# Kernel tuning notes

Hardware: AMD Instinct MI355X
Metric: run time of the kernel (lower is better)

The kernel has to match this reference:

```python
import jax, jax.numpy as jnp
import numpy as np

T, B, E, H, HID, SIG = 1024, 4, 1024, 16, 1024, 64


def setup_inputs() -> dict:
    key = jax.random.key(0)
    ks = jax.random.split(key, 16)
    sc = 0.02
    return {
        "x": jax.random.normal(ks[0], (T, B, E), jnp.float32),
        "Wq": jax.random.normal(ks[1], (E, E), jnp.float32) * sc,
        "bq": jnp.zeros((E,), jnp.float32),
        "Wk": jax.random.normal(ks[2], (E, E), jnp.float32) * sc,
        "bk": jnp.zeros((E,), jnp.float32),
        "Wv": jax.random.normal(ks[3], (E, E), jnp.float32) * sc,
        "bv": jnp.zeros((E,), jnp.float32),
        "Wo": jax.random.normal(ks[4], (E, E), jnp.float32) * sc,
        "bo": jnp.zeros((E,), jnp.float32),
        "W1": jax.random.normal(ks[5], (HID, E), jnp.float32) * sc,
        "b1": jnp.zeros((HID,), jnp.float32),
        "W2": jax.random.normal(ks[6], (SIG, HID), jnp.float32) * sc,
        "b2": jnp.zeros((SIG,), jnp.float32),
        "head_signatures": jax.random.normal(ks[7], (H, SIG), jnp.float32),
    }


def reference(x, Wq, bq, Wk, bk, Wv, bv, Wo, bo, W1, b1, W2, b2, head_signatures):
    # x: (T, B, E) fairseq layout; self-attention, no mask, eval mode (no dropout)
    T_, B_, E_ = x.shape
    H_ = head_signatures.shape[0]
    d = E_ // H_
    scaling = d ** -0.5

    q = (x @ Wq.T + bq) * scaling            # (T,B,E)
    k = x @ Wk.T + bk
    v = x @ Wv.T + bv

    def split_heads(z):                        # (T,B,E) -> (B,H,T,d)
        return z.reshape(T_, B_, H_, d).transpose(1, 2, 0, 3)

    qh, kh, vh = split_heads(q), split_heads(k), split_heads(v)

    scores = jnp.einsum("bhtd,bhsd->bhts", qh, kh)   # (B,H,T,T)
    attn = jax.nn.softmax(scores, axis=-1)
    o = jnp.einsum("bhts,bhsd->bhtd", attn, vh)      # (B,H,T,d)

    # head-competition gate: signature MLP on x, match against head signatures,
    # softmax over heads ('softmax' competition type)
    t = jax.nn.relu(x @ W1.T + b1) @ W2.T + b2       # (T,B,SIG)
    logits = t @ head_signatures.T                   # (T,B,H)
    gate = jax.nn.softmax(logits, axis=-1)
    gate = gate.transpose(1, 2, 0)                   # (B,H,T)

    o = o * gate[..., None]                          # gate per-head outputs
    out = o.transpose(2, 0, 1, 3).reshape(T_, B_, E_)  # (T,B,E)
    return out @ Wo.T + bo
```

## Files before the change

### kernel.cpp

```cpp
#include <hip/hip_runtime.h>

#define Tn   1024
#define Bn   4
#define En   1024
#define Hn   16
#define HIDn 1024
#define SIGn 64
#define Mn   (Tn * Bn)

typedef short  s8x8  __attribute__((ext_vector_type(8)));
typedef float  f32x4 __attribute__((ext_vector_type(4)));

__device__ __forceinline__ float bf2f(unsigned short u) {
    return __uint_as_float(((unsigned int)u) << 16);
}
__device__ __forceinline__ unsigned short f2bf(float f) {
    unsigned int x = __float_as_uint(f);
    unsigned int r = (x + 0x7fffu + ((x >> 16) & 1u)) >> 16;
    return (unsigned short)r;
}
__device__ __forceinline__ float exp2asm(float x) {
    float r;
    asm("v_exp_f32 %0, %1" : "=v"(r) : "v"(x));
    return r;
}
__device__ __forceinline__ unsigned int cvtpk(float a, float b) {
    unsigned int r;
    asm("v_cvt_pk_bf16_f32 %0, %1, %2" : "=v"(r) : "v"(a), "v"(b));
    return r;
}

__device__ __forceinline__ void gload_lds16(const void* g, void* l) {
    __builtin_amdgcn_global_load_lds(
        (const __attribute__((address_space(1))) unsigned int*)g,
        (__attribute__((address_space(3))) unsigned int*)l, 16, 0, 0);
}

__global__ __launch_bounds__(256) void cast_bf16(
    const float* __restrict__ s, unsigned short* __restrict__ d, int n8)
{
    int i = blockIdx.x * 256 + threadIdx.x;
    if (i >= n8) return;
    const float4* p = (const float4*)(s + (size_t)i * 8);
    float4 a = p[0], b = p[1];
    s8x8 o;
    o[0] = (short)f2bf(a.x); o[1] = (short)f2bf(a.y);
    o[2] = (short)f2bf(a.z); o[3] = (short)f2bf(a.w);
    o[4] = (short)f2bf(b.x); o[5] = (short)f2bf(b.y);
    o[6] = (short)f2bf(b.z); o[7] = (short)f2bf(b.w);
    *(s8x8*)(d + (size_t)i * 8) = o;
}

__global__ __launch_bounds__(256) void cast_w4(
    const float* __restrict__ W1, const float* __restrict__ Wq,
    const float* __restrict__ Wk, const float* __restrict__ Wv,
    unsigned short* __restrict__ Wcat)
{
    const size_t WELEM = (size_t)En * En;
    int y = blockIdx.y;
    const float* src = (y == 0) ? W1 : (y == 1) ? Wq : (y == 2) ? Wk : Wv;
    unsigned short* dst = Wcat + (size_t)y * WELEM;
    int i = blockIdx.x * 256 + threadIdx.x;
    const float4* p = (const float4*)(src + (size_t)i * 8);
    float4 a = p[0], b = p[1];
    s8x8 o;
    o[0] = (short)f2bf(a.x); o[1] = (short)f2bf(a.y);
    o[2] = (short)f2bf(a.z); o[3] = (short)f2bf(a.w);
    o[4] = (short)f2bf(b.x); o[5] = (short)f2bf(b.y);
    o[6] = (short)f2bf(b.z); o[7] = (short)f2bf(b.w);
    *(s8x8*)(dst + (size_t)i * 8) = o;
}

__global__ __launch_bounds__(256) void bias_concat(
    const float* __restrict__ b1, const float* __restrict__ bq,
    const float* __restrict__ bk, const float* __restrict__ bv,
    float* __restrict__ bcat)
{
    int i = blockIdx.x * 256 + threadIdx.x;
    int w = i >> 10;
    const float* s = (w == 0) ? b1 : (w == 1) ? bq : (w == 2) ? bk : bv;
    bcat[i] = s[i & 1023];
}

template <int PRE>
__global__ __launch_bounds__(256) void fused_proj(
    const float* __restrict__ X, const unsigned short* __restrict__ Xb,
    const unsigned short* __restrict__ Wcat, const float* __restrict__ bcat,
    unsigned short* __restrict__ t1b, unsigned short* __restrict__ qb,
    unsigned short* __restrict__ kb, unsigned short* __restrict__ vb)
{
    __shared__ __align__(16) short As[128 * 32];
    __shared__ __align__(16) short Bs[128 * 32];
    const int tid  = threadIdx.x;
    const int wave = tid >> 6;
    const int lane = tid & 63;
    const int ln15 = lane & 15;
    const int kq   = lane >> 4;
    const int wr   = wave >> 1;
    const int wc   = wave & 1;
    const int bn   = blockIdx.x;
    const int bm   = blockIdx.y;
    const size_t rowA0 = (size_t)bm * 128;
    const size_t rowB0 = (size_t)bn * 128;

    const int lrow   = lane >> 2;
    const int lchunk = lane & 3;

    f32x4 acc[4][4];
#pragma unroll
    for (int m = 0; m < 4; m++)
#pragma unroll
        for (int n = 0; n < 4; n++) acc[m][n] = (f32x4){0.f, 0.f, 0.f, 0.f};

    for (int k0 = 0; k0 < 1024; k0 += 32) {
#pragma unroll
        for (int i = 0; i < 2; i++) {
            int row = wave * 32 + i * 16 + lrow;
            int c   = lchunk ^ ((row >> 1) & 3);
            gload_lds16(Wcat + (rowB0 + row) * 1024 + k0 + c * 8,
                        &Bs[(wave * 32 + i * 16) * 32]);
        }
        if (PRE) {
#pragma unroll
            for (int i = 0; i < 2; i++) {
                int row = wave * 32 + i * 16 + lrow;
                int c   = lchunk ^ ((row >> 1) & 3);
                gload_lds16(Xb + (rowA0 + row) * 1024 + k0 + c * 8,
                            &As[(wave * 32 + i * 16) * 32]);
            }
        } else {
            const int srow = tid >> 1;
            const int scol = (tid & 1) * 16;
            const float4* src = (const float4*)(X + (rowA0 + srow) * 1024 + k0 + scol);
            float4 a = src[0], b = src[1], c4 = src[2], d4 = src[3];
            s8x8 v0, v1;
            v0[0] = (short)f2bf(a.x);  v0[1] = (short)f2bf(a.y);
            v0[2] = (short)f2bf(a.z);  v0[3] = (short)f2bf(a.w);
            v0[4] = (short)f2bf(b.x);  v0[5] = (short)f2bf(b.y);
            v0[6] = (short)f2bf(b.z);  v0[7] = (short)f2bf(b.w);
            v1[0] = (short)f2bf(c4.x); v1[1] = (short)f2bf(c4.y);
            v1[2] = (short)f2bf(c4.z); v1[3] = (short)f2bf(c4.w);
            v1[4] = (short)f2bf(d4.x); v1[5] = (short)f2bf(d4.y);
            v1[6] = (short)f2bf(d4.z); v1[7] = (short)f2bf(d4.w);
            int sw = (srow >> 1) & 3;
            int c0 = (scol >> 3) ^ sw;
            int c1 = ((scol >> 3) + 1) ^ sw;
            *(s8x8*)&As[srow * 32 + c0 * 8] = v0;
            *(s8x8*)&As[srow * 32 + c1 * 8] = v1;
        }
        asm volatile("s_waitcnt vmcnt(0)" ::: "memory");
        __syncthreads();

        s8x8 af[4], bf[4];
#pragma unroll
        for (int m = 0; m < 4; m++) {
            int row = wr * 64 + m * 16 + ln15;
            af[m] = *(const s8x8*)&As[row * 32 + (kq ^ ((row >> 1) & 3)) * 8];
        }
#pragma unroll
        for (int n = 0; n < 4; n++) {
            int row = wc * 64 + n * 16 + ln15;
            bf[n] = *(const s8x8*)&Bs[row * 32 + (kq ^ ((row >> 1) & 3)) * 8];
        }
#pragma unroll
        for (int m = 0; m < 4; m++)
#pragma unroll
            for (int n = 0; n < 4; n++)
                acc[m][n] = __builtin_amdgcn_mfma_f32_16x16x32_bf16(
                    af[m], bf[n], acc[m][n], 0, 0, 0);
        __syncthreads();
    }

    const int which = bn >> 3;
    unsigned short* dst = (which == 0) ? t1b : (which == 1) ? qb
                        : (which == 2) ? kb : vb;
    const float scale = (which == 1) ? 0.18033688011112042f : 1.0f;
    const int   relu  = (which == 0);
    const int   cbase = (bn & 7) * 128;

    float bcol[4];
#pragma unroll
    for (int n = 0; n < 4; n++)
        bcol[n] = bcat[bn * 128 + wc * 64 + n * 16 + ln15];
#pragma unroll
    for (int m = 0; m < 4; m++) {
        size_t gr0 = rowA0 + wr * 64 + m * 16 + kq * 4;
#pragma unroll
        for (int n = 0; n < 4; n++) {
            int gc = cbase + wc * 64 + n * 16 + ln15;
#pragma unroll
            for (int j = 0; j < 4; j++) {
                float vv = acc[m][n][j] + bcol[n];
                if (relu) vv = fmaxf(vv, 0.f);
                vv *= scale;
                dst[(gr0 + j) * 1024 + gc] = f2bf(vv);
            }
        }
    }
}

__global__ __launch_bounds__(256) void out_proj(
    const unsigned short* __restrict__ A, const unsigned short* __restrict__ W,
    const float* __restrict__ bias, float* __restrict__ C)
{
    __shared__ __align__(16) short As[64 * 32];
    __shared__ __align__(16) short Bs[128 * 32];
    const int tid  = threadIdx.x;
    const int wave = tid >> 6;
    const int lane = tid & 63;
    const int ln15 = lane & 15;
    const int kq   = lane >> 4;
    const int wr   = wave >> 1;
    const int wc   = wave & 1;
    const size_t rowA0 = (size_t)blockIdx.y * 64;
    const size_t rowB0 = (size_t)blockIdx.x * 128;

    const int lrow   = lane >> 2;
    const int lchunk = lane & 3;

    f32x4 acc[2][4];
#pragma unroll
    for (int m = 0; m < 2; m++)
#pragma unroll
        for (int n = 0; n < 4; n++) acc[m][n] = (f32x4){0.f, 0.f, 0.f, 0.f};

    for (int k0 = 0; k0 < 1024; k0 += 32) {
        {
            int row = wave * 16 + lrow;
            int c   = lchunk ^ ((row >> 1) & 3);
            gload_lds16(A + (rowA0 + row) * 1024 + k0 + c * 8,
                        &As[(wave * 16) * 32]);
        }
#pragma unroll
        for (int i = 0; i < 2; i++) {
            int row = wave * 32 + i * 16 + lrow;
            int c   = lchunk ^ ((row >> 1) & 3);
            gload_lds16(W + (rowB0 + row) * 1024 + k0 + c * 8,
                        &Bs[(wave * 32 + i * 16) * 32]);
        }
        asm volatile("s_waitcnt vmcnt(0)" ::: "memory");
        __syncthreads();

        s8x8 af[2], bf[4];
#pragma unroll
        for (int m = 0; m < 2; m++) {
            int row = wr * 32 + m * 16 + ln15;
            af[m] = *(const s8x8*)&As[row * 32 + (kq ^ ((row >> 1) & 3)) * 8];
        }
#pragma unroll
        for (int n = 0; n < 4; n++) {
            int row = wc * 64 + n * 16 + ln15;
            bf[n] = *(const s8x8*)&Bs[row * 32 + (kq ^ ((row >> 1) & 3)) * 8];
        }
#pragma unroll
        for (int m = 0; m < 2; m++)
#pragma unroll
            for (int n = 0; n < 4; n++)
                acc[m][n] = __builtin_amdgcn_mfma_f32_16x16x32_bf16(
                    af[m], bf[n], acc[m][n], 0, 0, 0);
        __syncthreads();
    }

    float bcol[4];
#pragma unroll
    for (int n = 0; n < 4; n++)
        bcol[n] = bias[rowB0 + wc * 64 + n * 16 + ln15];
#pragma unroll
    for (int m = 0; m < 2; m++) {
        size_t gr0 = rowA0 + wr * 32 + m * 16 + kq * 4;
#pragma unroll
        for (int n = 0; n < 4; n++) {
            size_t gc = rowB0 + wc * 64 + n * 16 + ln15;
#pragma unroll
            for (int j = 0; j < 4; j++)
                C[(gr0 + j) * 1024 + gc] = acc[m][n][j] + bcol[n];
        }
    }
}

__global__ __launch_bounds__(256) void t2gate(
    const unsigned short* __restrict__ t1, const unsigned short* __restrict__ W2b,
    const float* __restrict__ b2, const float* __restrict__ hs,
    float* __restrict__ gate)
{
    __shared__ __align__(16) short As[16 * 32];
    __shared__ __align__(16) short Bs[64 * 32];
    __shared__ float t2s[16][65];
    __shared__ float hss[16][65];
    const int tid  = threadIdx.x;
    const int wave = tid >> 6;
    const int lane = tid & 63;
    const int ln15 = lane & 15;
    const int kq   = lane >> 4;
    const int m0   = blockIdx.x * 16;

    {
        int r = tid >> 4, c = (tid & 15) * 4;
        float4 v = *(const float4*)(hs + r * 64 + c);
        hss[r][c] = v.x; hss[r][c + 1] = v.y; hss[r][c + 2] = v.z; hss[r][c + 3] = v.w;
    }

    f32x4 acc = (f32x4){0.f, 0.f, 0.f, 0.f};
    for (int k0 = 0; k0 < 1024; k0 += 32) {
        if (tid < 64) {
            int row = tid >> 2, ch = tid & 3;
            int cs = ch ^ ((row >> 1) & 3);
            s8x8 vA = *(const s8x8*)(t1 + (size_t)(m0 + row) * 1024 + k0 + ch * 8);
            *(s8x8*)&As[row * 32 + cs * 8] = vA;
        }
        {
            int row = tid >> 2, ch = tid & 3;
            int cs = ch ^ ((row >> 1) & 3);
            s8x8 vB = *(const s8x8*)(W2b + (size_t)row * 1024 + k0 + ch * 8);
            *(s8x8*)&Bs[row * 32 + cs * 8] = vB;
        }
        __syncthreads();
        int arow = ln15;
        int brow = wave * 16 + ln15;
        s8x8 af = *(const s8x8*)&As[arow * 32 + (kq ^ ((arow >> 1) & 3)) * 8];
        s8x8 bf = *(const s8x8*)&Bs[brow * 32 + (kq ^ ((brow >> 1) & 3)) * 8];
        acc = __builtin_amdgcn_mfma_f32_16x16x32_bf16(af, bf, acc, 0, 0, 0);
        __syncthreads();
    }

#pragma unroll
    for (int j = 0; j < 4; j++)
        t2s[kq * 4 + j][wave * 16 + ln15] = acc[j] + b2[wave * 16 + ln15];
    __syncthreads();

    int r = tid >> 4, hd = tid & 15;
    float s = 0.f;
#pragma unroll 16
    for (int d = 0; d < 64; d++) s += t2s[r][d] * hss[hd][d];
    float mx = s;
    mx = fmaxf(mx, __shfl_xor(mx, 1));
    mx = fmaxf(mx, __shfl_xor(mx, 2));
    mx = fmaxf(mx, __shfl_xor(mx, 4));
    mx = fmaxf(mx, __shfl_xor(mx, 8));
    float e = __expf(s - mx);
    float sum = e;
    sum += __shfl_xor(sum, 1);
    sum += __shfl_xor(sum, 2);
    sum += __shfl_xor(sum, 4);
    sum += __shfl_xor(sum, 8);
    gate[(size_t)(m0 + r) * Hn + hd] = e / sum;
}

__global__ __launch_bounds__(256) void transpose_v(
    const unsigned short* __restrict__ vb, unsigned short* __restrict__ vt)
{
    __shared__ unsigned short ts[64][65];
    const int bh = blockIdx.x;
    const int b = bh >> 4, h = bh & 15;
    const int t0 = blockIdx.y * 64;
    const int tid = threadIdx.x;
    {
        int tr = tid >> 2, dq = (tid & 3) * 16;
        const unsigned short* src =
            vb + ((size_t)(t0 + tr) * Bn + b) * En + h * 64 + dq;
        s8x8 a = *(const s8x8*)src;
        s8x8 c = *(const s8x8*)(src + 8);
#pragma unroll
        for (int i = 0; i < 8; i++) {
            ts[tr][dq + i]     = (unsigned short)a[i];
            ts[tr][dq + 8 + i] = (unsigned short)c[i];
        }
    }
    __syncthreads();
    {
        int dr = tid >> 2, tq = (tid & 3) * 16;
        unsigned short* dst = vt + ((size_t)bh * 64 + dr) * Tn + t0 + tq;
        s8x8 o0, o1;
#pragma unroll
        for (int i = 0; i < 8; i++) {
            o0[i] = (short)ts[tq + i][dr];
            o1[i] = (short)ts[tq + 8 + i][dr];
        }
        *(s8x8*)dst = o0;
        *(s8x8*)(dst + 8) = o1;
    }
}

__global__ __launch_bounds__(256, 5) void attn_mfma(
    const unsigned short* __restrict__ q, const unsigned short* __restrict__ k,
    const unsigned short* __restrict__ vt, const float* __restrict__ gate,
    unsigned short* __restrict__ o)
{
    __shared__ __align__(16) short Kls[2][64 * 64];
    __shared__ __align__(16) short Vls[2][64 * 64];

    const int tid  = threadIdx.x;
    const int w    = tid >> 6;
    const int lane = tid & 63;
    const int ln   = lane & 15;
    const int kq   = lane >> 4;
    const int bh   = blockIdx.x;
    const int b    = bh >> 4;
    const int h    = bh & 15;
    const int qt   = blockIdx.y;

    s8x8 qf[2];
    {
        const int qrow = qt * 64 + w * 16 + ln;
        const unsigned short* src =
            q + ((size_t)qrow * Bn + b) * En + h * 64 + kq * 8;
        qf[0] = *(const s8x8*)(src);
        qf[1] = *(const s8x8*)(src + 32);
    }

    f32x4 OT[4];
#pragma unroll
    for (int n = 0; n < 4; n++) OT[n] = (f32x4){0.f, 0.f, 0.f, 0.f};
    float mrun = -1e30f, lrun = 0.f;

    const int srow0 = w * 16 + (lane >> 3);

    auto stage = [&](int bufi, int s0) {
#pragma unroll
        for (int i = 0; i < 2; i++) {
            int row = srow0 + i * 8;
            int c   = (lane & 7) ^ (row & 7);
            int sK  = 32 * (w >> 1) + 4 * (w & 1)
                    + 8 * ((row >> 2) & 3) + (row & 3);
            const unsigned short* gk =
                k + ((size_t)(s0 + sK) * Bn + b) * En + h * 64 + c * 8;
            gload_lds16(gk, &Kls[bufi][w * 1024 + i * 512]);
            const unsigned short* gv =
                vt + ((size_t)bh * 64 + row) * Tn + s0 + c * 8;
            gload_lds16(gv, &Vls[bufi][w * 1024 + i * 512]);
        }
    };

    stage(0, 0);
    asm volatile("s_waitcnt vmcnt(0)" ::: "memory");
    __syncthreads();

    int cur = 0;
    for (int t = 0; t < Tn / 64; t++) {
        if (t + 1 < Tn / 64) stage(cur ^ 1, (t + 1) * 64);

        f32x4 S[4];
#pragma unroll
        for (int n = 0; n < 4; n++) {
            S[n] = (f32x4){0.f, 0.f, 0.f, 0.f};
#pragma unroll
            for (int kk = 0; kk < 2; kk++) {
                int row = n * 16 + ln;
                int cc  = (kk * 4 + kq) ^ (row & 7);
                s8x8 kf = *(const s8x8*)&Kls[cur][row * 64 + cc * 8];
                S[n] = __builtin_amdgcn_mfma_f32_16x16x32_bf16(kf, qf[kk], S[n], 0, 0, 0);
            }
        }

        float rm;
        {
            f32x4 t0 = S[0];
#pragma unroll
            for (int n = 1; n < 4; n++) {
                t0[0] = fmaxf(t0[0], S[n][0]); t0[1] = fmaxf(t0[1], S[n][1]);
                t0[2] = fmaxf(t0[2], S[n][2]); t0[3] = fmaxf(t0[3], S[n][3]);
            }
            rm = fmaxf(fmaxf(t0[0], t0[1]), fmaxf(t0[2], t0[3]));
            rm = fmaxf(rm, __shfl_xor(rm, 16));
            rm = fmaxf(rm, __shfl_xor(rm, 32));
        }

        if (__any(rm > mrun + 8.0f)) {
            float mnew = fmaxf(mrun, rm);
            float fs = exp2asm(mrun - mnew);
            lrun *= fs;
#pragma unroll
            for (int n = 0; n < 4; n++) {
                OT[n][0] *= fs; OT[n][1] *= fs; OT[n][2] *= fs; OT[n][3] *= fs;
            }
            mrun = mnew;
        }

        float ps = 0.f;
#pragma unroll
        for (int n = 0; n < 4; n++) {
            S[n][0] = exp2asm(S[n][0] - mrun); ps += S[n][0];
            S[n][1] = exp2asm(S[n][1] - mrun); ps += S[n][1];
            S[n][2] = exp2asm(S[n][2] - mrun); ps += S[n][2];
            S[n][3] = exp2asm(S[n][3] - mrun); ps += S[n][3];
        }
        ps += __shfl_xor(ps, 16);
        ps += __shfl_xor(ps, 32);
        lrun += ps;

        union { unsigned int u[4]; s8x8 v; } pb[2];
#pragma unroll
        for (int kk = 0; kk < 2; kk++) {
            pb[kk].u[0] = cvtpk(S[2 * kk][0],     S[2 * kk][1]);
            pb[kk].u[1] = cvtpk(S[2 * kk][2],     S[2 * kk][3]);
            pb[kk].u[2] = cvtpk(S[2 * kk + 1][0], S[2 * kk + 1][1]);
            pb[kk].u[3] = cvtpk(S[2 * kk + 1][2], S[2 * kk + 1][3]);
        }

#pragma unroll
        for (int kk = 0; kk < 2; kk++) {
#pragma unroll
            for (int n = 0; n < 4; n++) {
                int row = n * 16 + ln;
                int cv  = (kk * 4 + kq) ^ (row & 7);
                s8x8 vf = *(const s8x8*)&Vls[cur][row * 64 + cv * 8];
                OT[n] = __builtin_amdgcn_mfma_f32_16x16x32_bf16(vf, pb[kk].v, OT[n], 0, 0, 0);
            }
        }

        asm volatile("s_waitcnt vmcnt(0)" ::: "memory");
        __syncthreads();
        cur ^= 1;
    }

    {
        int tq = qt * 64 + w * 16 + ln;
        size_t m = (size_t)tq * Bn + b;
        float g = gate[m * Hn + h] / lrun;
        unsigned short* dst = o + m * En + h * 64;
#pragma unroll
        for (int n = 0; n < 4; n++) {
            int d0 = n * 16 + kq * 4;
            uint2 pkv;
            pkv.x = cvtpk(OT[n][0] * g, OT[n][1] * g);
            pkv.y = cvtpk(OT[n][2] * g, OT[n][3] * g);
            *(uint2*)(dst + d0) = pkv;
        }
    }
}

extern "C" void kernel_launch(void* const* d_in, const int* in_sizes, int n_in,
                              void* d_out, int out_size, void* d_ws, size_t ws_size,
                              hipStream_t stream)
{
    const float* x  = (const float*)d_in[0];
    const float* Wq = (const float*)d_in[1];
    const float* bq = (const float*)d_in[2];
    const float* Wk = (const float*)d_in[3];
    const float* bk = (const float*)d_in[4];
    const float* Wv = (const float*)d_in[5];
    const float* bv = (const float*)d_in[6];
    const float* Wo = (const float*)d_in[7];
    const float* bo = (const float*)d_in[8];
    const float* W1 = (const float*)d_in[9];
    const float* b1 = (const float*)d_in[10];
    const float* W2 = (const float*)d_in[11];
    const float* b2 = (const float*)d_in[12];
    const float* hs = (const float*)d_in[13];

    const size_t WELEM = (size_t)En * En;
    unsigned short* Wcat = (unsigned short*)d_ws;
    unsigned short* W2b  = Wcat + 4 * WELEM;
    float* bcat = (float*)(W2b + (size_t)SIGn * HIDn);
    float* gate = bcat + 4096;
    unsigned short* t1b = (unsigned short*)(gate + (size_t)Mn * Hn);
    unsigned short* qb  = t1b + (size_t)Mn * En;
    unsigned short* kb  = qb  + (size_t)Mn * En;
    unsigned short* vb  = kb  + (size_t)Mn * En;
    unsigned short* xb  = vb  + (size_t)Mn * En;
    unsigned short* Wob = Wcat;
    unsigned short* vtb = t1b;
    unsigned short* ob  = vb;

    const size_t need_xb =
        (size_t)((char*)(xb + (size_t)Mn * En) - (char*)d_ws);
    const bool pre = ws_size >= need_xb;

    dim3 blk(256);
    const int castGrid = (int)(WELEM / 8 / 256);

    cast_w4<<<dim3(castGrid, 4), blk, 0, stream>>>(W1, Wq, Wk, Wv, Wcat);
    cast_bf16<<<32, blk, 0, stream>>>(W2, W2b, (int)((size_t)SIGn * HIDn / 8));
    bias_concat<<<16, blk, 0, stream>>>(b1, bq, bk, bv, bcat);

    if (pre) {
        cast_bf16<<<dim3((int)((size_t)Mn * En / 8 / 256)), blk, 0, stream>>>(
            x, xb, (int)((size_t)Mn * En / 8));
        fused_proj<1><<<dim3(32, 32), blk, 0, stream>>>(
            x, xb, Wcat, bcat, t1b, qb, kb, vb);
    } else {
        fused_proj<0><<<dim3(32, 32), blk, 0, stream>>>(
            x, xb, Wcat, bcat, t1b, qb, kb, vb);
    }

    t2gate<<<dim3(Mn / 16), blk, 0, stream>>>(t1b, W2b, b2, hs, gate);

    transpose_v<<<dim3(Bn * Hn, Tn / 64), blk, 0, stream>>>(vb, vtb);

    cast_bf16<<<castGrid, blk, 0, stream>>>(Wo, Wob, (int)(WELEM / 8));

    attn_mfma<<<dim3(Bn * Hn, Tn / 64), blk, 0, stream>>>(qb, kb, vtb, gate, ob);

    out_proj<<<dim3(En / 128, Mn / 64), blk, 0, stream>>>(ob, Wob, bo, (float*)d_out);
}
```

Measured before the change: 141.3 us.

## Double GEMM K-tile depth, swizzle workgroup order, prioritize MFMA waves in attention

The fused projection, output projection and t2gate GEMMs now stage K tiles of 64 instead of 32 per iteration, using an 8-chunk XOR LDS swizzle. This halves the number of barrier/wait rounds per GEMM at the cost of twice the LDS per block. Workgroup IDs are remapped into an XCD-aware order to improve L2 reuse of shared A/B tiles across chiplets. t2gate switches from register-staged copies to direct global-to-LDS loads. The attention kernel raises wave priority around its MFMA sections.

```diff
diff --git a/kernel.cpp b/kernel.cpp
--- a/kernel.cpp
+++ b/kernel.cpp
@@ -89,85 +89,87 @@
     unsigned short* __restrict__ t1b, unsigned short* __restrict__ qb,
     unsigned short* __restrict__ kb, unsigned short* __restrict__ vb)
 {
-    __shared__ __align__(16) short As[128 * 32];
-    __shared__ __align__(16) short Bs[128 * 32];
-    const int tid  = threadIdx.x;
-    const int wave = tid >> 6;
-    const int lane = tid & 63;
-    const int ln15 = lane & 15;
-    const int kq   = lane >> 4;
-    const int wr   = wave >> 1;
-    const int wc   = wave & 1;
-    const int bn   = blockIdx.x;
-    const int bm   = blockIdx.y;
+    __shared__ __align__(16) short As[128 * 64];
+    __shared__ __align__(16) short Bs[128 * 64];
+    const int tid   = threadIdx.x;
+    const int wave  = tid >> 6;
+    const int lane  = tid & 63;
+    const int ln15  = lane & 15;
+    const int kq    = lane >> 4;
+    const int wr    = wave >> 1;
+    const int wc    = wave & 1;
+    const int lrow8 = lane >> 3;
+    const int lch   = lane & 7;
+
+    const int wgid = blockIdx.y * 32 + blockIdx.x;
+    const int swz  = (wgid & 7) * 128 + (wgid >> 3);
+    const int bn   = swz & 31;
+    const int bm   = swz >> 5;
     const size_t rowA0 = (size_t)bm * 128;
     const size_t rowB0 = (size_t)bn * 128;
 
-    const int lrow   = lane >> 2;
-    const int lchunk = lane & 3;
-
     f32x4 acc[4][4];
 #pragma unroll
     for (int m = 0; m < 4; m++)
 #pragma unroll
         for (int n = 0; n < 4; n++) acc[m][n] = (f32x4){0.f, 0.f, 0.f, 0.f};
 
-    for (int k0 = 0; k0 < 1024; k0 += 32) {
-#pragma unroll
-        for (int i = 0; i < 2; i++) {
-            int row = wave * 32 + i * 16 + lrow;
-            int c   = lchunk ^ ((row >> 1) & 3);
-            gload_lds16(Wcat + (rowB0 + row) * 1024 + k0 + c * 8,
-                        &Bs[(wave * 32 + i * 16) * 32]);
+    for (int k0 = 0; k0 < 1024; k0 += 64) {
+#pragma unroll
+        for (int i = 0; i < 4; i++) {
+            int row = wave * 32 + i * 8 + lrow8;
+            int cg  = lch ^ (row & 7);
+            gload_lds16(Wcat + (rowB0 + row) * 1024 + k0 + cg * 8,
+                        &Bs[(wave * 32 + i * 8) * 64]);
         }
         if (PRE) {
 #pragma unroll
-            for (int i = 0; i < 2; i++) {
-                int row = wave * 32 + i * 16 + lrow;
-                int c   = lchunk ^ ((row >> 1) & 3);
-                gload_lds16(Xb + (rowA0 + row) * 1024 + k0 + c * 8,
-                            &As[(wave * 32 + i * 16) * 32]);
+            for (int i = 0; i < 4; i++) {
+                int row = wave * 32 + i * 8 + lrow8;
+                int cg  = lch ^ (row & 7);
+                gload_lds16(Xb + (rowA0 + row) * 1024 + k0 + cg * 8,
+                            &As[(wave * 32 + i * 8) * 64]);
             }
         } else {
             const int srow = tid >> 1;
-            const int scol = (tid & 1) * 16;
-            const float4* src = (const float4*)(X + (rowA0 + srow) * 1024 + k0 + scol);
-            float4 a = src[0], b = src[1], c4 = src[2], d4 = src[3];
-            s8x8 v0, v1;
-            v0[0] = (short)f2bf(a.x);  v0[1] = (short)f2bf(a.y);
-            v0[2] = (short)f2bf(a.z);  v0[3] = (short)f2bf(a.w);
-            v0[4] = (short)f2bf(b.x);  v0[5] = (short)f2bf(b.y);
-            v0[6] = (short)f2bf(b.z);  v0[7] = (short)f2bf(b.w);
-            v1[0] = (short)f2bf(c4.x); v1[1] = (short)f2bf(c4.y);
-            v1[2] = (short)f2bf(c4.z); v1[3] = (short)f2bf(c4.w);
-            v1[4] = (short)f2bf(d4.x); v1[5] = (short)f2bf(d4.y);
-            v1[6] = (short)f2bf(d4.z); v1[7] = (short)f2bf(d4.w);
-            int sw = (srow >> 1) & 3;
-            int c0 = (scol >> 3) ^ sw;
-            int c1 = ((scol >> 3) + 1) ^ sw;
-            *(s8x8*)&As[srow * 32 + c0 * 8] = v0;
-            *(s8x8*)&As[srow * 32 + c1 * 8] = v1;
+            const int scol = (tid & 1) * 32;
+            const float4* src =
+                (const float4*)(X + (rowA0 + srow) * 1024 + k0 + scol);
+#pragma unroll
+            for (int j = 0; j < 4; j++) {
+                float4 a = src[2 * j], b = src[2 * j + 1];
+                s8x8 v;
+                v[0] = (short)f2bf(a.x); v[1] = (short)f2bf(a.y);
+                v[2] = (short)f2bf(a.z); v[3] = (short)f2bf(a.w);
+                v[4] = (short)f2bf(b.x); v[5] = (short)f2bf(b.y);
+                v[6] = (short)f2bf(b.z); v[7] = (short)f2bf(b.w);
+                int cs = ((scol >> 3) + j) ^ (srow & 7);
+                *(s8x8*)&As[srow * 64 + cs * 8] = v;
+            }
         }
         asm volatile("s_waitcnt vmcnt(0)" ::: "memory");
         __syncthreads();
 
-        s8x8 af[4], bf[4];
-#pragma unroll
-        for (int m = 0; m < 4; m++) {
-            int row = wr * 64 + m * 16 + ln15;
-            af[m] = *(const s8x8*)&As[row * 32 + (kq ^ ((row >> 1) & 3)) * 8];
-        }
-#pragma unroll
-        for (int n = 0; n < 4; n++) {
-            int row = wc * 64 + n * 16 + ln15;
-            bf[n] = *(const s8x8*)&Bs[row * 32 + (kq ^ ((row >> 1) & 3)) * 8];
-        }
-#pragma unroll
-        for (int m = 0; m < 4; m++)
-#pragma unroll
-            for (int n = 0; n < 4; n++)
-                acc[m][n] = __builtin_amdgcn_mfma_f32_16x16x32_bf16(
-                    af[m], bf[n], acc[m][n], 0, 0, 0);
+#pragma unroll
+        for (int kk = 0; kk < 2; kk++) {
+            s8x8 af[4], bf4[4];
+#pragma unroll
+            for (int m = 0; m < 4; m++) {
+                int row = wr * 64 + m * 16 + ln15;
+                af[m] = *(const s8x8*)&As[row * 64 + (((kk * 4 + kq) ^ (row & 7)) * 8)];
+            }
+#pragma unroll
+            for (int n = 0; n < 4; n++) {
+                int row = wc * 64 + n * 16 + ln15;
+                bf4[n] = *(const s8x8*)&Bs[row * 64 + (((kk * 4 + kq) ^ (row & 7)) * 8)];
+            }
+#pragma unroll
+            for (int m = 0; m < 4; m++)
+#pragma unroll
+                for (int n = 0; n < 4; n++)
+                    acc[m][n] = __builtin_amdgcn_mfma_f32_16x16x32_bf16(
+                        af[m], bf4[n], acc[m][n], 0, 0, 0);
+        }
         __syncthreads();
     }
 
@@ -203,20 +205,24 @@
     const unsigned short* __restrict__ A, const unsigned short* __restrict__ W,
     const float* __restrict__ bias, float* __restrict__ C)
 {
-    __shared__ __align__(16) short As[64 * 32];
-    __shared__ __align__(16) short Bs[128 * 32];
-    const int tid  = threadIdx.x;
-    const int wave = tid >> 6;
-    const int lane = tid & 63;
-    const int ln15 = lane & 15;
-    const int kq   = lane >> 4;
-    const int wr   = wave >> 1;
-    const int wc   = wave & 1;
-    const size_t rowA0 = (size_t)blockIdx.y * 64;
-    const size_t rowB0 = (size_t)blockIdx.x * 128;
-
-    const int lrow   = lane >> 2;
-    const int lchunk = lane & 3;
+    __shared__ __align__(16) short As[64 * 64];
+    __shared__ __align__(16) short Bs[128 * 64];
+    const int tid   = threadIdx.x;
+    const int wave  = tid >> 6;
+    const int lane  = tid & 63;
+    const int ln15  = lane & 15;
+    const int kq    = lane >> 4;
+    const int wr    = wave >> 1;
+    const int wc    = wave & 1;
+    const int lrow8 = lane >> 3;
+    const int lch   = lane & 7;
+
+    const int wgid = blockIdx.y * 8 + blockIdx.x;
+    const int swz  = (wgid & 7) * 64 + (wgid >> 3);
+    const int bx   = swz & 7;
+    const int by   = swz >> 3;
+    const size_t rowA0 = (size_t)by * 64;
+    const size_t rowB0 = (size_t)bx * 128;
 
     f32x4 acc[2][4];
 #pragma unroll
@@ -224,40 +230,44 @@
 #pragma unroll
         for (int n = 0; n < 4; n++) acc[m][n] = (f32x4){0.f, 0.f, 0.f, 0.f};
 
-    for (int k0 = 0; k0 < 1024; k0 += 32) {
-        {
-            int row = wave * 16 + lrow;
-            int c   = lchunk ^ ((row >> 1) & 3);
-            gload_lds16(A + (rowA0 + row) * 1024 + k0 + c * 8,
-                        &As[(wave * 16) * 32]);
-        }
+    for (int k0 = 0; k0 < 1024; k0 += 64) {
 #pragma unroll
         for (int i = 0; i < 2; i++) {
-            int row = wave * 32 + i * 16 + lrow;
-            int c   = lchunk ^ ((row >> 1) & 3);
-            gload_lds16(W + (rowB0 + row) * 1024 + k0 + c * 8,
-                        &Bs[(wave * 32 + i * 16) * 32]);
+            int row = wave * 16 + i * 8 + lrow8;
+            int cg  = lch ^ (row & 7);
+            gload_lds16(A + (rowA0 + row) * 1024 + k0 + cg * 8,
+                        &As[(wave * 16 + i * 8) * 64]);
+        }
+#pragma unroll
+        for (int i = 0; i < 4; i++) {
+            int row = wave * 32 + i * 8 + lrow8;
+            int cg  = lch ^ (row & 7);
+            gload_lds16(W + (rowB0 + row) * 1024 + k0 + cg * 8,
+                        &Bs[(wave * 32 + i * 8) * 64]);
         }
         asm volatile("s_waitcnt vmcnt(0)" ::: "memory");
         __syncthreads();
 
-        s8x8 af[2], bf[4];
-#pragma unroll
-        for (int m = 0; m < 2; m++) {
-            int row = wr * 32 + m * 16 + ln15;
-            af[m] = *(const s8x8*)&As[row * 32 + (kq ^ ((row >> 1) & 3)) * 8];
-        }
-#pragma unroll
-        for (int n = 0; n < 4; n++) {
-            int row = wc * 64 + n * 16 + ln15;
-            bf[n] = *(const s8x8*)&Bs[row * 32 + (kq ^ ((row >> 1) & 3)) * 8];
-        }
-#pragma unroll
-        for (int m = 0; m < 2; m++)
-#pragma unroll
-            for (int n = 0; n < 4; n++)
-                acc[m][n] = __builtin_amdgcn_mfma_f32_16x16x32_bf16(
-                    af[m], bf[n], acc[m][n], 0, 0, 0);
+#pragma unroll
+        for (int kk = 0; kk < 2; kk++) {
+            s8x8 af[2], bf4[4];
+#pragma unroll
+            for (int m = 0; m < 2; m++) {
+                int row = wr * 32 + m * 16 + ln15;
+                af[m] = *(const s8x8*)&As[row * 64 + (((kk * 4 + kq) ^ (row & 7)) * 8)];
+            }
+#pragma unroll
+            for (int n = 0; n < 4; n++) {
+                int row = wc * 64 + n * 16 + ln15;
+                bf4[n] = *(const s8x8*)&Bs[row * 64 + (((kk * 4 + kq) ^ (row & 7)) * 8)];
+            }
+#pragma unroll
+            for (int m = 0; m < 2; m++)
+#pragma unroll
+                for (int n = 0; n < 4; n++)
+                    acc[m][n] = __builtin_amdgcn_mfma_f32_16x16x32_bf16(
+                        af[m], bf4[n], acc[m][n], 0, 0, 0);
+        }
         __syncthreads();
     }
 
@@ -283,16 +293,18 @@
     const float* __restrict__ b2, const float* __restrict__ hs,
     float* __restrict__ gate)
 {
-    __shared__ __align__(16) short As[16 * 32];
-    __shared__ __align__(16) short Bs[64 * 32];
+    __shared__ __align__(16) short As[16 * 64];
+    __shared__ __align__(16) short Bs[64 * 64];
     __shared__ float t2s[16][65];
     __shared__ float hss[16][65];
-    const int tid  = threadIdx.x;
-    const int wave = tid >> 6;
-    const int lane = tid & 63;
-    const int ln15 = lane & 15;
-    const int kq   = lane >> 4;
-    const int m0   = blockIdx.x * 16;
+    const int tid   = threadIdx.x;
+    const int wave  = tid >> 6;
+    const int lane  = tid & 63;
+    const int ln15  = lane & 15;
+    const int kq    = lane >> 4;
+    const int lrow8 = lane >> 3;
+    const int lch   = lane & 7;
+    const int m0    = blockIdx.x * 16;
 
     {
         int r = tid >> 4, c = (tid & 15) * 4;
@@ -301,25 +313,31 @@
     }
 
     f32x4 acc = (f32x4){0.f, 0.f, 0.f, 0.f};
-    for (int k0 = 0; k0 < 1024; k0 += 32) {
-        if (tid < 64) {
-            int row = tid >> 2, ch = tid & 3;
-            int cs = ch ^ ((row >> 1) & 3);
-            s8x8 vA = *(const s8x8*)(t1 + (size_t)(m0 + row) * 1024 + k0 + ch * 8);
-            *(s8x8*)&As[row * 32 + cs * 8] = vA;
-        }
-        {
-            int row = tid >> 2, ch = tid & 3;
-            int cs = ch ^ ((row >> 1) & 3);
-            s8x8 vB = *(const s8x8*)(W2b + (size_t)row * 1024 + k0 + ch * 8);
-            *(s8x8*)&Bs[row * 32 + cs * 8] = vB;
-        }
+    for (int k0 = 0; k0 < 1024; k0 += 64) {
+        if (wave < 2) {
+            int row = wave * 8 + lrow8;
+            int cg  = lch ^ (row & 7);
+            gload_lds16(t1 + (size_t)(m0 + row) * 1024 + k0 + cg * 8,
+                        &As[(wave * 8) * 64]);
+        }
+#pragma unroll
+        for (int i = 0; i < 2; i++) {
+            int row = wave * 16 + i * 8 + lrow8;
+            int cg  = lch ^ (row & 7);
+            gload_lds16(W2b + (size_t)row * 1024 + k0 + cg * 8,
+                        &Bs[(wave * 16 + i * 8) * 64]);
+        }
+        asm volatile("s_waitcnt vmcnt(0)" ::: "memory");
         __syncthreads();
-        int arow = ln15;
-        int brow = wave * 16 + ln15;
-        s8x8 af = *(const s8x8*)&As[arow * 32 + (kq ^ ((arow >> 1) & 3)) * 8];
-        s8x8 bf = *(const s8x8*)&Bs[brow * 32 + (kq ^ ((brow >> 1) & 3)) * 8];
-        acc = __builtin_amdgcn_mfma_f32_16x16x32_bf16(af, bf, acc, 0, 0, 0);
+
+#pragma unroll
+        for (int kk = 0; kk < 2; kk++) {
+            int arow = ln15;
+            int brow = wave * 16 + ln15;
+            s8x8 af = *(const s8x8*)&As[arow * 64 + (((kk * 4 + kq) ^ (arow & 7)) * 8)];
+            s8x8 bf = *(const s8x8*)&Bs[brow * 64 + (((kk * 4 + kq) ^ (brow & 7)) * 8)];
+            acc = __builtin_amdgcn_mfma_f32_16x16x32_bf16(af, bf, acc, 0, 0, 0);
+        }
         __syncthreads();
     }
 
@@ -440,6 +458,7 @@
         if (t + 1 < Tn / 64) stage(cur ^ 1, (t + 1) * 64);
 
         f32x4 S[4];
+        __builtin_amdgcn_s_setprio(1);
 #pragma unroll
         for (int n = 0; n < 4; n++) {
             S[n] = (f32x4){0.f, 0.f, 0.f, 0.f};
@@ -451,6 +470,7 @@
                 S[n] = __builtin_amdgcn_mfma_f32_16x16x32_bf16(kf, qf[kk], S[n], 0, 0, 0);
             }
         }
+        __builtin_amdgcn_s_setprio(0);
 
         float rm;
         {
@@ -497,6 +517,7 @@
             pb[kk].u[3] = cvtpk(S[2 * kk + 1][2], S[2 * kk + 1][3]);
         }
 
+        __builtin_amdgcn_s_setprio(1);
 #pragma unroll
         for (int kk = 0; kk < 2; kk++) {
 #pragma unroll
@@ -507,6 +528,7 @@
                 OT[n] = __builtin_amdgcn_mfma_f32_16x16x32_bf16(vf, pb[kk].v, OT[n], 0, 0, 0);
             }
         }
+        __builtin_amdgcn_s_setprio(0);
 
         asm volatile("s_waitcnt vmcnt(0)" ::: "memory");
         __syncthreads();
@@ -591,5 +613,5 @@
 
     attn_mfma<<<dim3(Bn * Hn, Tn / 64), blk, 0, stream>>>(qb, kb, vtb, gate, ob);
 
-    out_proj<<<dim3(En / 128, Mn / 64), blk, 0, stream>>>(ob, Wob, bo, (float*)d_out);
-}
+    out_proj<<<dim3(8, 64), blk, 0, stream>>>(ob, Wob, bo, (float*)d_out);
+}
```

New measurement: 135.3 us. 1.04x faster.

## Double-buffer LDS in projection GEMMs, widen t2gate K-step, add MFMA priority hints

Applied to the files above, without the earlier changes.

The fused QKV/MLP projection and the output projection now use two LDS buffers, so the next K-slice is prefetched while MFMAs run on the current one. This replaces the old load-wait-compute-sync loop per step. The t2gate kernel now loads 64-wide K tiles with direct global-to-LDS loads and an 8-way swizzle, which halves its loop iterations. The attention kernel wraps its MFMA blocks in s_setprio to favour matrix issue. In exchange, LDS use in the GEMMs doubles, which may cut occupancy, and the fp32 X path in fused_proj still converts through registers.

```diff
diff --git a/kernel.cpp b/kernel.cpp
--- a/kernel.cpp
+++ b/kernel.cpp
@@ -89,8 +89,8 @@
     unsigned short* __restrict__ t1b, unsigned short* __restrict__ qb,
     unsigned short* __restrict__ kb, unsigned short* __restrict__ vb)
 {
-    __shared__ __align__(16) short As[128 * 32];
-    __shared__ __align__(16) short Bs[128 * 32];
+    __shared__ __align__(16) short As[2][128 * 32];
+    __shared__ __align__(16) short Bs[2][128 * 32];
     const int tid  = threadIdx.x;
     const int wave = tid >> 6;
     const int lane = tid & 63;
@@ -98,40 +98,41 @@
     const int kq   = lane >> 4;
     const int wr   = wave >> 1;
     const int wc   = wave & 1;
-    const int bn   = blockIdx.x;
-    const int bm   = blockIdx.y;
+    const int lrow = lane >> 2;
+    const int lch  = lane & 3;
+
+    const int bn = blockIdx.x;
+    const int bm = blockIdx.y;
     const size_t rowA0 = (size_t)bm * 128;
     const size_t rowB0 = (size_t)bn * 128;
 
-    const int lrow   = lane >> 2;
-    const int lchunk = lane & 3;
-
     f32x4 acc[4][4];
 #pragma unroll
     for (int m = 0; m < 4; m++)
 #pragma unroll
         for (int n = 0; n < 4; n++) acc[m][n] = (f32x4){0.f, 0.f, 0.f, 0.f};
 
-    for (int k0 = 0; k0 < 1024; k0 += 32) {
+    auto stage = [&](int buf, int k0) {
 #pragma unroll
         for (int i = 0; i < 2; i++) {
             int row = wave * 32 + i * 16 + lrow;
-            int c   = lchunk ^ ((row >> 1) & 3);
+            int c   = lch ^ ((row >> 1) & 3);
             gload_lds16(Wcat + (rowB0 + row) * 1024 + k0 + c * 8,
-                        &Bs[(wave * 32 + i * 16) * 32]);
+                        &Bs[buf][(wave * 32 + i * 16) * 32]);
         }
         if (PRE) {
 #pragma unroll
             for (int i = 0; i < 2; i++) {
                 int row = wave * 32 + i * 16 + lrow;
-                int c   = lchunk ^ ((row >> 1) & 3);
+                int c   = lch ^ ((row >> 1) & 3);
                 gload_lds16(Xb + (rowA0 + row) * 1024 + k0 + c * 8,
-                            &As[(wave * 32 + i * 16) * 32]);
+                            &As[buf][(wave * 32 + i * 16) * 32]);
             }
         } else {
             const int srow = tid >> 1;
             const int scol = (tid & 1) * 16;
-            const float4* src = (const float4*)(X + (rowA0 + srow) * 1024 + k0 + scol);
+            const float4* src =
+                (const float4*)(X + (rowA0 + srow) * 1024 + k0 + scol);
             float4 a = src[0], b = src[1], c4 = src[2], d4 = src[3];
             s8x8 v0, v1;
             v0[0] = (short)f2bf(a.x);  v0[1] = (short)f2bf(a.y);
@@ -145,30 +146,40 @@
             int sw = (srow >> 1) & 3;
             int c0 = (scol >> 3) ^ sw;
             int c1 = ((scol >> 3) + 1) ^ sw;
-            *(s8x8*)&As[srow * 32 + c0 * 8] = v0;
-            *(s8x8*)&As[srow * 32 + c1 * 8] = v1;
-        }
+            *(s8x8*)&As[buf][srow * 32 + c0 * 8] = v0;
+            *(s8x8*)&As[buf][srow * 32 + c1 * 8] = v1;
+        }
+    };
+
+    stage(0, 0);
+    asm volatile("s_waitcnt vmcnt(0)" ::: "memory");
+    __syncthreads();
+
+    int cur = 0;
+    for (int t = 0; t < 32; t++) {
+        if (t + 1 < 32) stage(cur ^ 1, (t + 1) * 32);
+
+        s8x8 af[4], bf4[4];
+#pragma unroll
+        for (int m = 0; m < 4; m++) {
+            int row = wr * 64 + m * 16 + ln15;
+            af[m] = *(const s8x8*)&As[cur][row * 32 + ((kq ^ ((row >> 1) & 3)) * 8)];
+        }
+#pragma unroll
+        for (int n = 0; n < 4; n++) {
+            int row = wc * 64 + n * 16 + ln15;
+            bf4[n] = *(const s8x8*)&Bs[cur][row * 32 + ((kq ^ ((row >> 1) & 3)) * 8)];
+        }
+#pragma unroll
+        for (int m = 0; m < 4; m++)
+#pragma unroll
+            for (int n = 0; n < 4; n++)
+                acc[m][n] = __builtin_amdgcn_mfma_f32_16x16x32_bf16(
+                    af[m], bf4[n], acc[m][n], 0, 0, 0);
+
         asm volatile("s_waitcnt vmcnt(0)" ::: "memory");
         __syncthreads();
-
-        s8x8 af[4], bf[4];
-#pragma unroll
-        for (int m = 0; m < 4; m++) {
-            int row = wr * 64 + m * 16 + ln15;
-            af[m] = *(const s8x8*)&As[row * 32 + (kq ^ ((row >> 1) & 3)) * 8];
-        }
-#pragma unroll
-        for (int n = 0; n < 4; n++) {
-            int row = wc * 64 + n * 16 + ln15;
-            bf[n] = *(const s8x8*)&Bs[row * 32 + (kq ^ ((row >> 1) & 3)) * 8];
-        }
-#pragma unroll
-        for (int m = 0; m < 4; m++)
-#pragma unroll
-            for (int n = 0; n < 4; n++)
-                acc[m][n] = __builtin_amdgcn_mfma_f32_16x16x32_bf16(
-                    af[m], bf[n], acc[m][n], 0, 0, 0);
-        __syncthreads();
+        cur ^= 1;
     }
 
     const int which = bn >> 3;
@@ -203,8 +214,8 @@
     const unsigned short* __restrict__ A, const unsigned short* __restrict__ W,
     const float* __restrict__ bias, float* __restrict__ C)
 {
-    __shared__ __align__(16) short As[64 * 32];
-    __shared__ __align__(16) short Bs[128 * 32];
+    __shared__ __align__(16) short As[2][64 * 32];
+    __shared__ __align__(16) short Bs[2][128 * 32];
     const int tid  = threadIdx.x;
     const int wave = tid >> 6;
     const int lane = tid & 63;
@@ -212,53 +223,63 @@
     const int kq   = lane >> 4;
     const int wr   = wave >> 1;
     const int wc   = wave & 1;
+    const int lrow = lane >> 2;
+    const int lch  = lane & 3;
+
     const size_t rowA0 = (size_t)blockIdx.y * 64;
     const size_t rowB0 = (size_t)blockIdx.x * 128;
 
-    const int lrow   = lane >> 2;
-    const int lchunk = lane & 3;
-
     f32x4 acc[2][4];
 #pragma unroll
     for (int m = 0; m < 2; m++)
 #pragma unroll
         for (int n = 0; n < 4; n++) acc[m][n] = (f32x4){0.f, 0.f, 0.f, 0.f};
 
-    for (int k0 = 0; k0 < 1024; k0 += 32) {
+    auto stage = [&](int buf, int k0) {
         {
             int row = wave * 16 + lrow;
-            int c   = lchunk ^ ((row >> 1) & 3);
+            int c   = lch ^ ((row >> 1) & 3);
             gload_lds16(A + (rowA0 + row) * 1024 + k0 + c * 8,
-                        &As[(wave * 16) * 32]);
+                        &As[buf][(wave * 16) * 32]);
         }
 #pragma unroll
         for (int i = 0; i < 2; i++) {
             int row = wave * 32 + i * 16 + lrow;
-            int c   = lchunk ^ ((row >> 1) & 3);
+            int c   = lch ^ ((row >> 1) & 3);
             gload_lds16(W + (rowB0 + row) * 1024 + k0 + c * 8,
-                        &Bs[(wave * 32 + i * 16) * 32]);
-        }
+                        &Bs[buf][(wave * 32 + i * 16) * 32]);
+        }
+    };
+
+    stage(0, 0);
+    asm volatile("s_waitcnt vmcnt(0)" ::: "memory");
+    __syncthreads();
+
+    int cur = 0;
+    for (int t = 0; t < 32; t++) {
+        if (t + 1 < 32) stage(cur ^ 1, (t + 1) * 32);
+
+        s8x8 af[2], bf4[4];
+#pragma unroll
+        for (int m = 0; m < 2; m++) {
+            int row = wr * 32 + m * 16 + ln15;
+            af[m] = *(const s8x8*)&As[cur][row * 32 + ((kq ^ ((row >> 1) & 3)) * 8)];
+        }
+#pragma unroll
+        for (int n = 0; n < 4; n++) {
+            int row = wc * 64 + n * 16 + ln15;
+            bf4[n] = *(const s8x8*)&Bs[cur][row * 32 + ((kq ^ ((row >> 1) & 3)) * 8)];
+        }
+#pragma unroll
+        for (int m = 0; m < 2; m++)
+#pragma unroll
+            for (int n = 0; n < 4; n++)
+                acc[m][n] = __builtin_amdgcn_mfma_f32_16x16x32_bf16(
+                    af[m], bf4[n], acc[m][n], 0, 0, 0);
+
         asm volatile("s_waitcnt vmcnt(0)" ::: "memory");
         __syncthreads();
-
-        s8x8 af[2], bf[4];
-#pragma unroll
-        for (int m = 0; m < 2; m++) {
-            int row = wr * 32 + m * 16 + ln15;
-            af[m] = *(const s8x8*)&As[row * 32 + (kq ^ ((row >> 1) & 3)) * 8];
-        }
-#pragma unroll
-        for (int n = 0; n < 4; n++) {
-            int row = wc * 64 + n * 16 + ln15;
-            bf[n] = *(const s8x8*)&Bs[row * 32 + (kq ^ ((row >> 1) & 3)) * 8];
-        }
-#pragma unroll
-        for (int m = 0; m < 2; m++)
-#pragma unroll
-            for (int n = 0; n < 4; n++)
-                acc[m][n] = __builtin_amdgcn_mfma_f32_16x16x32_bf16(
-                    af[m], bf[n], acc[m][n], 0, 0, 0);
-        __syncthreads();
+        cur ^= 1;
     }
 
     float bcol[4];
@@ -283,16 +304,18 @@
     const float* __restrict__ b2, const float* __restrict__ hs,
     float* __restrict__ gate)
 {
-    __shared__ __align__(16) short As[16 * 32];
-    __shared__ __align__(16) short Bs[64 * 32];
+    __shared__ __align__(16) short As[16 * 64];
+    __shared__ __align__(16) short Bs[64 * 64];
     __shared__ float t2s[16][65];
     __shared__ float hss[16][65];
-    const int tid  = threadIdx.x;
-    const int wave = tid >> 6;
-    const int lane = tid & 63;
-    const int ln15 = lane & 15;
-    const int kq   = lane >> 4;
-    const int m0   = blockIdx.x * 16;
+    const int tid   = threadIdx.x;
+    const int wave  = tid >> 6;
+    const int lane  = tid & 63;
+    const int ln15  = lane & 15;
+    const int kq    = lane >> 4;
+    const int lrow8 = lane >> 3;
+    const int lch   = lane & 7;
+    const int m0    = blockIdx.x * 16;
 
     {
         int r = tid >> 4, c = (tid & 15) * 4;
@@ -301,25 +324,31 @@
     }
 
     f32x4 acc = (f32x4){0.f, 0.f, 0.f, 0.f};
-    for (int k0 = 0; k0 < 1024; k0 += 32) {
-        if (tid < 64) {
-            int row = tid >> 2, ch = tid & 3;
-            int cs = ch ^ ((row >> 1) & 3);
-            s8x8 vA = *(const s8x8*)(t1 + (size_t)(m0 + row) * 1024 + k0 + ch * 8);
-            *(s8x8*)&As[row * 32 + cs * 8] = vA;
-        }
-        {
-            int row = tid >> 2, ch = tid & 3;
-            int cs = ch ^ ((row >> 1) & 3);
-            s8x8 vB = *(const s8x8*)(W2b + (size_t)row * 1024 + k0 + ch * 8);
-            *(s8x8*)&Bs[row * 32 + cs * 8] = vB;
-        }
+    for (int k0 = 0; k0 < 1024; k0 += 64) {
+        if (wave < 2) {
+            int row = wave * 8 + lrow8;
+            int cg  = lch ^ (row & 7);
+            gload_lds16(t1 + (size_t)(m0 + row) * 1024 + k0 + cg * 8,
+                        &As[(wave * 8) * 64]);
+        }
+#pragma unroll
+        for (int i = 0; i < 2; i++) {
+            int row = wave * 16 + i * 8 + lrow8;
+            int cg  = lch ^ (row & 7);
+            gload_lds16(W2b + (size_t)row * 1024 + k0 + cg * 8,
+                        &Bs[(wave * 16 + i * 8) * 64]);
+        }
+        asm volatile("s_waitcnt vmcnt(0)" ::: "memory");
         __syncthreads();
-        int arow = ln15;
-        int brow = wave * 16 + ln15;
-        s8x8 af = *(const s8x8*)&As[arow * 32 + (kq ^ ((arow >> 1) & 3)) * 8];
-        s8x8 bf = *(const s8x8*)&Bs[brow * 32 + (kq ^ ((brow >> 1) & 3)) * 8];
-        acc = __builtin_amdgcn_mfma_f32_16x16x32_bf16(af, bf, acc, 0, 0, 0);
+
+#pragma unroll
+        for (int kk = 0; kk < 2; kk++) {
+            int arow = ln15;
+            int brow = wave * 16 + ln15;
+            s8x8 af = *(const s8x8*)&As[arow * 64 + (((kk * 4 + kq) ^ (arow & 7)) * 8)];
+            s8x8 bf = *(const s8x8*)&Bs[brow * 64 + (((kk * 4 + kq) ^ (brow & 7)) * 8)];
+            acc = __builtin_amdgcn_mfma_f32_16x16x32_bf16(af, bf, acc, 0, 0, 0);
+        }
         __syncthreads();
     }
 
@@ -440,6 +469,7 @@
         if (t + 1 < Tn / 64) stage(cur ^ 1, (t + 1) * 64);
 
         f32x4 S[4];
+        __builtin_amdgcn_s_setprio(1);
 #pragma unroll
         for (int n = 0; n < 4; n++) {
             S[n] = (f32x4){0.f, 0.f, 0.f, 0.f};
@@ -451,6 +481,7 @@
                 S[n] = __builtin_amdgcn_mfma_f32_16x16x32_bf16(kf, qf[kk], S[n], 0, 0, 0);
             }
         }
+        __builtin_amdgcn_s_setprio(0);
 
         float rm;
         {
@@ -497,6 +528,7 @@
             pb[kk].u[3] = cvtpk(S[2 * kk + 1][2], S[2 * kk + 1][3]);
         }
 
+        __builtin_amdgcn_s_setprio(1);
 #pragma unroll
         for (int kk = 0; kk < 2; kk++) {
 #pragma unroll
@@ -507,6 +539,7 @@
                 OT[n] = __builtin_amdgcn_mfma_f32_16x16x32_bf16(vf, pb[kk].v, OT[n], 0, 0, 0);
             }
         }
+        __builtin_amdgcn_s_setprio(0);
 
         asm volatile("s_waitcnt vmcnt(0)" ::: "memory");
         __syncthreads();
@@ -591,5 +624,5 @@
 
     attn_mfma<<<dim3(Bn * Hn, Tn / 64), blk, 0, stream>>>(qb, kb, vtb, gate, ob);
 
-    out_proj<<<dim3(En / 128, Mn / 64), blk, 0, stream>>>(ob, Wob, bo, (float*)d_out);
-}
+    out_proj<<<dim3(8, 64), blk, 0, stream>>>(ob, Wob, bo, (float*)d_out);
+}
```

Result: slower. 157.9 us (+11.8%).
